# Performance work log

Measured on AMD Instinct MI355X. Metric: run time of the kernel, lower is better.

The kernel has to match this reference:

```python
import jax, jax.numpy as jnp
import numpy as np
from jax import lax

B, N, C, FH, FW = 2, 6, 64, 16, 44
D = 64
DEPTH_MIN, DEPTH_MAX = 1.0, 60.0
IMG_H, IMG_W = 256, 704
BEV_H, BEV_W = 128, 128
XMIN, XMAX = -51.2, 51.2
YMIN, YMAX = -51.2, 51.2
BN_EPS = 1e-5


def _make_cameras():
    fx = fy = 557.0
    K = np.array([[fx, 0.0, IMG_W / 2.0], [0.0, fy, IMG_H / 2.0], [0.0, 0.0, 1.0]], np.float32)
    intr = np.broadcast_to(K, (B, N, 3, 3)).copy()
    extr = np.zeros((B, N, 4, 4), np.float32)
    for n in range(N):
        c, s = np.cos(2 * np.pi * n / N), np.sin(2 * np.pi * n / N)
        # columns = [right, down, forward] of camera expressed in ego frame
        Rc = np.array([[s, 0.0, c], [-c, 0.0, s], [0.0, -1.0, 0.0]], np.float32)
        extr[:, n, :3, :3] = Rc
        extr[:, n, :3, 3] = np.array([c, s, 1.5], np.float32)
        extr[:, n, 3, 3] = 1.0
    return jnp.asarray(intr), jnp.asarray(extr)


def _frustum():
    # (D, FH, FW, 3) holding (u*d, v*d, d) in original-image pixel coords
    ds = jnp.linspace(DEPTH_MIN, DEPTH_MAX, D)[:, None, None]
    xs = jnp.linspace(0.0, IMG_W - 1.0, FW)[None, None, :]
    ys = jnp.linspace(0.0, IMG_H - 1.0, FH)[None, :, None]
    d = jnp.broadcast_to(ds, (D, FH, FW))
    x = jnp.broadcast_to(xs, (D, FH, FW))
    y = jnp.broadcast_to(ys, (D, FH, FW))
    return jnp.stack([x * d, y * d, d], axis=-1)


def _conv(x, w, b, pad):
    y = lax.conv_general_dilated(x, w, (1, 1), pad, dimension_numbers=("NCHW", "OIHW", "NCHW"))
    return y + b[None, :, None, None]


def setup_inputs() -> dict:
    key = jax.random.key(0)
    k0, k1, k2 = jax.random.split(key, 3)
    intr, extr = _make_cameras()
    return {
        "features": jax.random.normal(k0, (B, N, C, FH, FW), jnp.float32),
        "intrinsics": intr,
        "extrinsics": extr,
        "conv1_w": jax.random.normal(k1, (C, C, 3, 3), jnp.float32) / np.sqrt(C * 9.0).astype(np.float32),
        "conv1_b": jnp.zeros((C,), jnp.float32),
        "bn_gamma": jnp.ones((C,), jnp.float32),
        "bn_beta": jnp.zeros((C,), jnp.float32),
        "bn_mean": jnp.zeros((C,), jnp.float32),
        "bn_var": jnp.ones((C,), jnp.float32),
        "conv2_w": jax.random.normal(k2, (D, C, 1, 1), jnp.float32) / np.sqrt(float(C)).astype(np.float32),
        "conv2_b": jnp.zeros((D,), jnp.float32),
    }


def reference(features, intrinsics, extrinsics, conv1_w, conv1_b, bn_gamma, bn_beta, bn_mean, bn_var, conv2_w, conv2_b):
    Bv, Nv, Cv, fH, fW = features.shape
    x = features.reshape(Bv * Nv, Cv, fH, fW)

    # DepthNet: conv3x3 -> BN (inference form) -> ReLU -> conv1x1 -> softmax over depth bins
    h = _conv(x, conv1_w, conv1_b, "SAME")
    scale = (bn_gamma / jnp.sqrt(bn_var + BN_EPS))[None, :, None, None]
    h = (h - bn_mean[None, :, None, None]) * scale + bn_beta[None, :, None, None]
    h = jax.nn.relu(h)
    depth = jax.nn.softmax(_conv(h, conv2_w, conv2_b, "VALID"), axis=1)  # (B*N, D, fH, fW)

    # Lift: outer product of features with depth distribution
    volume = x[:, :, None] * depth[:, None]  # (B*N, C, D, fH, fW)

    # Unproject frustum to ego frame for every camera
    pts = _frustum()  # (D, fH, fW, 3)
    Kinv = jnp.linalg.inv(intrinsics)  # (B, N, 3, 3)
    cam = jnp.einsum("bnij,dhwj->bndhwi", Kinv, pts)
    R = extrinsics[..., :3, :3]
    t = extrinsics[..., :3, 3]
    ego = jnp.einsum("bnij,bndhwj->bndhwi", R, cam) + t[:, :, None, None, None, :]

    # BEV voxel indices; invalid points routed to an overflow bucket that is dropped
    ix = jnp.floor((ego[..., 0] - XMIN) / (XMAX - XMIN) * BEV_W).astype(jnp.int32)
    iy = jnp.floor((ego[..., 1] - YMIN) / (YMAX - YMIN) * BEV_H).astype(jnp.int32)
    valid = (ix >= 0) & (ix < BEV_W) & (iy >= 0) & (iy < BEV_H)
    idx = jnp.where(valid, iy * BEV_W + ix, BEV_H * BEV_W)  # (B, N, D, fH, fW)

    # Splat: scatter-add over all cameras/depths/pixels per batch element
    vol = volume.reshape(Bv, Nv, Cv, -1).transpose(0, 2, 1, 3).reshape(Bv, Cv, -1)  # (B, C, N*D*fH*fW)
    idxb = idx.reshape(Bv, -1)

    def pool(v, i):
        return jnp.zeros((Cv, BEV_H * BEV_W + 1), v.dtype).at[:, i].add(v)[:, :-1]

    return jax.vmap(pool)(vol, idxb).reshape(Bv, Cv, BEV_H, BEV_W)
```

## Files before the change

### kernel.cpp

```cpp
#include <hip/hip_runtime.h>
#include <hip/hip_bf16.h>
#include <math.h>

#define B_  2
#define N_  6
#define C_  64
#define FH_ 16
#define FW_ 44
#define D_  64
#define PIX (FH_*FW_)
#define BNI (B_*N_)
#define NPILLAR (BNI*PIX)
#define NPOINT (NPILLAR*D_)
#define BEVH 128
#define BEVW 128
#define BEVC (BEVH*BEVW)
#define NCELL (B_*BEVC)
#define PW 46
#define PP (18*PW)

typedef unsigned int u32;

__device__ __forceinline__ int rlane_i(int v, int l) {
    return __builtin_amdgcn_readlane(v, l);
}
__device__ __forceinline__ float rlane_f(float v, int l) {
    return __int_as_float(__builtin_amdgcn_readlane(__float_as_int(v), l));
}

__global__ __launch_bounds__(256) void k_init_conv(const float* __restrict__ feat,
                                                   const float* __restrict__ w1,
                                                   float* __restrict__ hpAll,
                                                   float* __restrict__ x_t,
                                                   const float* __restrict__ w2,
                                                   float* __restrict__ w2t,
                                                   u32* __restrict__ counts,
                                                   u32* __restrict__ gcursor,
                                                   const float* __restrict__ intr,
                                                   const float* __restrict__ extr,
                                                   double* __restrict__ Mbuf) {
    const int blk = blockIdx.x;
    const int tid = threadIdx.x;

    __shared__ float smem[16 * PP];

    if (blk < 768) {
        if (blk < 128) counts[blk * 256 + tid] = 0u;

        const int bn = blk >> 6;
        const int ch = (blk >> 4) & 3;
        const int o0 = (blk & 15) * 4;
        const int c0 = ch * 16;

        for (int t = tid; t < 4 * PP; t += 256)
            ((float4*)smem)[t] = make_float4(0.f, 0.f, 0.f, 0.f);
        __syncthreads();

        const float4* fb4 = (const float4*)(feat + ((size_t)bn * C_ + c0) * PIX);
#pragma unroll
        for (int k = 0; k < 11; ++k) {
            const int j = k * 256 + tid;
            const int pl = j / 176;
            const int r  = j % 176;
            const int row = r / 11, q = r % 11;
            const float4 v = fb4[j];
            float* dstp = &smem[pl * PP + (row + 1) * PW + q * 4 + 1];
            dstp[0] = v.x; dstp[1] = v.y; dstp[2] = v.z; dstp[3] = v.w;
        }
        __syncthreads();

        const int y0 = tid / FW_,          x0 = tid % FW_;
        const int y1 = (tid + 256) / FW_,  x1 = (tid + 256) % FW_;
        const int y2 = (tid + 512) / FW_,  x2 = (tid + 512) % FW_;
        const int rp0 = y0 * PW + x0;
        const int rp1 = y1 * PW + x1;
        const int rp2 = y2 * PW + x2;

        float a00=0,a01=0,a02=0,a03=0, a10=0,a11=0,a12=0,a13=0,
              a20=0,a21=0,a22=0,a23=0;
#pragma unroll 4
        for (int i = 0; i < 16; ++i) {
            const float* wr0 = w1 + ((size_t)(o0 + 0) * C_ + c0 + i) * 9;
            const float* wr1 = w1 + ((size_t)(o0 + 1) * C_ + c0 + i) * 9;
            const float* wr2 = w1 + ((size_t)(o0 + 2) * C_ + c0 + i) * 9;
            const float* wr3 = w1 + ((size_t)(o0 + 3) * C_ + c0 + i) * 9;
            const float* pb = &smem[i * PP];
#define CONV_SLOT(RP, A0, A1, A2, A3)                                          \
    {                                                                          \
        const float* bb = pb + (RP);                                           \
        const float n0=bb[0], n1=bb[1], n2=bb[2];                              \
        const float n3=bb[PW], n4=bb[PW+1], n5=bb[PW+2];                       \
        const float n6=bb[2*PW], n7=bb[2*PW+1], n8=bb[2*PW+2];                 \
        A0 += n0*wr0[0]+n1*wr0[1]+n2*wr0[2]+n3*wr0[3]+n4*wr0[4]                \
            + n5*wr0[5]+n6*wr0[6]+n7*wr0[7]+n8*wr0[8];                         \
        A1 += n0*wr1[0]+n1*wr1[1]+n2*wr1[2]+n3*wr1[3]+n4*wr1[4]                \
            + n5*wr1[5]+n6*wr1[6]+n7*wr1[7]+n8*wr1[8];                         \
        A2 += n0*wr2[0]+n1*wr2[1]+n2*wr2[2]+n3*wr2[3]+n4*wr2[4]                \
            + n5*wr2[5]+n6*wr2[6]+n7*wr2[7]+n8*wr2[8];                         \
        A3 += n0*wr3[0]+n1*wr3[1]+n2*wr3[2]+n3*wr3[3]+n4*wr3[4]                \
            + n5*wr3[5]+n6*wr3[6]+n7*wr3[7]+n8*wr3[8];                         \
    }
            CONV_SLOT(rp0, a00, a01, a02, a03);
            CONV_SLOT(rp1, a10, a11, a12, a13);
            if (tid < PIX - 512) CONV_SLOT(rp2, a20, a21, a22, a23);
#undef CONV_SLOT
        }
        float* hp = hpAll + (size_t)ch * NPOINT + (size_t)bn * PIX * C_;
        *(float4*)&hp[(size_t)tid * C_ + o0]         = make_float4(a00,a01,a02,a03);
        *(float4*)&hp[(size_t)(tid + 256) * C_ + o0] = make_float4(a10,a11,a12,a13);
        if (tid < PIX - 512)
            *(float4*)&hp[(size_t)(tid + 512) * C_ + o0] = make_float4(a20,a21,a22,a23);
    } else if (blk < 900) {
        const int u  = blk - 768;
        const int bn = u / 11;
        const int p0 = (u % 11) * 64;
        const int lane = tid & 63;
        const int row4 = tid >> 6;
        float* tile = smem;
#pragma unroll
        for (int k = 0; k < 16; ++k) {
            const int c = k * 4 + row4;
            tile[c * 65 + lane] = feat[((size_t)bn * C_ + c) * PIX + p0 + lane];
        }
        __syncthreads();
#pragma unroll
        for (int k = 0; k < 16; ++k) {
            const int r = k * 4 + row4;
            x_t[((size_t)bn * PIX + p0 + r) * C_ + lane] = tile[lane * 65 + r];
        }
    } else {
#pragma unroll
        for (int k = 0; k < 16; ++k) {
            const int idx = k * 256 + tid;
            const int d = idx >> 6, c = idx & 63;
            w2t[c * D_ + d] = w2[idx];
        }
        if (tid == 0) *gcursor = 0u;
        if (tid < BNI) {
            const float* K = &intr[tid * 9];
            const double a00 = K[0], a01 = K[1], a02 = K[2];
            const double a10 = K[3], a11 = K[4], a12 = K[5];
            const double a20 = K[6], a21 = K[7], a22 = K[8];
            const double det = a00 * (a11 * a22 - a12 * a21)
                             - a01 * (a10 * a22 - a12 * a20)
                             + a02 * (a10 * a21 - a11 * a20);
            const double id = 1.0 / det;
            double inv[9];
            inv[0] = (a11 * a22 - a12 * a21) * id;
            inv[1] = (a02 * a21 - a01 * a22) * id;
            inv[2] = (a01 * a12 - a02 * a11) * id;
            inv[3] = (a12 * a20 - a10 * a22) * id;
            inv[4] = (a00 * a22 - a02 * a20) * id;
            inv[5] = (a02 * a10 - a00 * a12) * id;
            inv[6] = (a10 * a21 - a11 * a20) * id;
            inv[7] = (a01 * a20 - a00 * a21) * id;
            inv[8] = (a00 * a11 - a01 * a10) * id;
            const float* E = &extr[tid * 16];
            double* M = &Mbuf[tid * 9];
            for (int r = 0; r < 3; ++r) {
                const double r0 = E[r*4+0], r1 = E[r*4+1], r2 = E[r*4+2];
                M[r*3+0] = r0*inv[0] + r1*inv[3] + r2*inv[6];
                M[r*3+1] = r0*inv[1] + r1*inv[4] + r2*inv[7];
                M[r*3+2] = r0*inv[2] + r1*inv[5] + r2*inv[8];
            }
        }
    }
}

__global__ __launch_bounds__(256) void k_depth(const float* __restrict__ hpAll,
                                               const float* __restrict__ b1,
                                               const float* __restrict__ gma,
                                               const float* __restrict__ bta,
                                               const float* __restrict__ mu,
                                               const float* __restrict__ var,
                                               const float* __restrict__ w2t,
                                               const float* __restrict__ b2,
                                               const double* __restrict__ Mbuf,
                                               const float* __restrict__ extr,
                                               uint2* __restrict__ pc,
                                               u32* __restrict__ counts) {
    const int wv = threadIdx.x >> 6;
    const int d  = threadIdx.x & 63;
    const int pillar = blockIdx.x * 4 + wv;
    const int bn = pillar / PIX;
    const int p  = pillar % PIX;
    const int yi = p / FW_;
    const int xi = p % FW_;

    __shared__ float hs[4][C_];
    {
        const size_t o = (size_t)pillar * C_ + d;
        float h = hpAll[o] + hpAll[NPOINT + o] + hpAll[2 * (size_t)NPOINT + o]
                + hpAll[3 * (size_t)NPOINT + o] + b1[d];
        const float sc = gma[d] / sqrtf(var[d] + 1e-5f);
        h = (h - mu[d]) * sc + bta[d];
        hs[wv][d] = h > 0.f ? h : 0.f;
    }
    __syncthreads();

    float logit = b2[d];
#pragma unroll
    for (int c = 0; c < C_; ++c) logit += hs[wv][c] * w2t[c * D_ + d];

    float m = logit;
#pragma unroll
    for (int off = 32; off; off >>= 1) m = fmaxf(m, __shfl_xor(m, off));
    float e = expf(logit - m);
    float s = e;
#pragma unroll
    for (int off = 32; off; off >>= 1) s += __shfl_xor(s, off);

    const double* M = &Mbuf[bn * 9];
    const double xn = (double)xi * (703.0 / 43.0);
    const double yn = (double)yi * 17.0;
    const double vx = M[0] * xn + M[1] * yn + M[2];
    const double vy = M[3] * xn + M[4] * yn + M[5];
    const double dd = 1.0 + (double)d * (59.0 / 63.0);
    const float* E = &extr[bn * 16];
    const double ex = dd * vx + (double)E[3];
    const double ey = dd * vy + (double)E[7];
    const int ix = (int)floor((ex + 51.2) * 1.25);
    const int iy = (int)floor((ey + 51.2) * 1.25);
    const bool valid = (ix >= 0) && (ix < BEVW) && (iy >= 0) && (iy < BEVH);

    const int i = pillar * D_ + d;
    uint2 rec;
    rec.x = __float_as_uint(e / s);
    if (valid) {
        const int cell = (bn / N_) * BEVC + iy * BEVW + ix;
        const u32 rank = atomicAdd(&counts[cell], 1u);
        rec.y = (rank << 15) | (u32)cell;
    } else {
        rec.y = 0xFFFFFFFFu;
    }
    pc[i] = rec;
}

__global__ __launch_bounds__(256) void k_alloc(const u32* __restrict__ counts,
                                               u32* __restrict__ offs,
                                               u32* __restrict__ gcursor) {
    const int cell = blockIdx.x * 256 + threadIdx.x;
    const int lane = threadIdx.x & 63;
    const u32 len = counts[cell];
    u32 incl = len;
#pragma unroll
    for (int off = 1; off < 64; off <<= 1) {
        u32 t = __shfl_up(incl, off);
        if (lane >= off) incl += t;
    }
    u32 base = 0;
    if (lane == 63) base = atomicAdd(gcursor, incl);
    base = (u32)__shfl((int)base, 63);
    offs[cell] = base + incl - len;
}

__global__ __launch_bounds__(256) void k_zero_place(const uint2* __restrict__ pc,
                                                    const u32* __restrict__ offs,
                                                    const u32* __restrict__ counts,
                                                    const u32* __restrict__ gcursor,
                                                    uint2* __restrict__ sorted,
                                                    u32* __restrict__ offs_end,
                                                    float* __restrict__ out) {
    const int blk = blockIdx.x;
    const int tid = threadIdx.x;
    if (blk < 2048) {
        const int gt = blk * 256 + tid;
        const int c4 = gt & 4095;
        const int bc = gt >> 12;
        const int b  = bc >> 6;
        const int cellbase = b * BEVC + (c4 << 2);
        const uint4 s4 = *(const uint4*)&offs[cellbase];
        const uint4 n4 = *(const uint4*)&counts[cellbase];
        float* dst = out + ((size_t)bc * BEVC) + (c4 << 2);
        if ((n4.x | n4.y | n4.z | n4.w) == 0u) {
            *(float4*)dst = make_float4(0.f, 0.f, 0.f, 0.f);
        } else {
            if (n4.x == 0u || (s4.x >> 6) != ((s4.x + n4.x - 1) >> 6)) dst[0] = 0.f;
            if (n4.y == 0u || (s4.y >> 6) != ((s4.y + n4.y - 1) >> 6)) dst[1] = 0.f;
            if (n4.z == 0u || (s4.z >> 6) != ((s4.z + n4.z - 1) >> 6)) dst[2] = 0.f;
            if (n4.w == 0u || (s4.w >> 6) != ((s4.w + n4.w - 1) >> 6)) dst[3] = 0.f;
        }
    } else if (blk < 4160) {
        const int i = (blk - 2048) * 256 + tid;
        const uint2 rec = pc[i];
        if (rec.y != 0xFFFFFFFFu) {
            const u32 cell = rec.y & 0x7FFFu;
            const u32 rank = rec.y >> 15;
            const u32 pos  = offs[cell] + rank;
            uint2 o; o.x = rec.x; o.y = (cell << 14) | (u32)(i >> 6);
            sorted[pos] = o;
        }
    } else {
        const u32 total = *gcursor;
        if (tid < 128) {
            uint2 dummy; dummy.x = 0u; dummy.y = 0xFFFFFFFFu;
            sorted[total + tid] = dummy;
        }
        if (tid == 128) *offs_end = total;
    }
}

__global__ __launch_bounds__(256) void k_pool(const uint2* __restrict__ sorted,
                                              const u32* __restrict__ offsets,
                                              const float* __restrict__ x_t,
                                              float* __restrict__ out) {
    const u32 P = offsets[NCELL];
    const int wv   = threadIdx.x >> 6;
    const int lane = threadIdx.x & 63;
    const u32 j0   = ((u32)blockIdx.x * 4u + (u32)wv) * 64u;
    if (j0 >= P) return;

    const uint2 pr  = sorted[j0 + (u32)lane];
    const float myw = __uint_as_float(pr.x);
    const int mycell = (int)(pr.y >> 14);
    int mypil = (int)(pr.y & 0x3FFFu);
    if (mypil >= NPILLAR) mypil = 0;

    const int prev_cell = (j0 > 0) ? (int)(sorted[j0 - 1].y >> 14) : -1;
    const int next_cell = (int)(sorted[j0 + 64].y >> 14);

    const int upc = __shfl_up(mycell, 1);
    const unsigned long long bm = __ballot(lane == 0 || mycell != upc);

    float xr[8];
#pragma unroll
    for (int t = 0; t < 8; ++t)
        xr[t] = x_t[(size_t)rlane_i(mypil, t) * C_ + lane];

    float acc = 0.f;
    bool first = true;

#pragma unroll
    for (int t = 0; t < 64; ++t) {
        acc += rlane_f(myw, t) * xr[t & 7];
        if (t + 8 < 64)
            xr[t & 7] = x_t[(size_t)rlane_i(mypil, t + 8) * C_ + lane];
        const bool flush = (t == 63) || ((bm >> (t + 1)) & 1ull);
        if (flush) {
            const int cc = rlane_i(mycell, t);
            if (cc < NCELL) {
                float* dst = out + ((size_t)(cc >> 14) * C_ + lane) * BEVC
                           + (cc & (BEVC - 1));
                const bool spans = (first && cc == prev_cell)
                                || (t == 63 && next_cell == cc);
                if (spans) atomicAdd(dst, acc);
                else *dst = acc;
            }
            acc = 0.f;
            first = false;
        }
    }
}

extern "C" void kernel_launch(void* const* d_in, const int* in_sizes, int n_in,
                              void* d_out, int out_size, void* d_ws, size_t ws_size,
                              hipStream_t stream) {
    const float* feat  = (const float*)d_in[0];
    const float* intr  = (const float*)d_in[1];
    const float* extr  = (const float*)d_in[2];
    const float* w1    = (const float*)d_in[3];
    const float* b1    = (const float*)d_in[4];
    const float* gma   = (const float*)d_in[5];
    const float* bta   = (const float*)d_in[6];
    const float* mu    = (const float*)d_in[7];
    const float* var   = (const float*)d_in[8];
    const float* w2    = (const float*)d_in[9];
    const float* b2    = (const float*)d_in[10];
    float* out = (float*)d_out;

    double* Mbuf    = (double*)d_ws;
    u32*    gcursor = (u32*)((char*)d_ws + 960);
    uint2*  sorted  = (uint2*)((char*)d_ws + 1024);
    uint2*  pc      = sorted + NPOINT + 128;
    float*  x_t     = (float*)(pc + NPOINT);
    float*  hpAll   = x_t + NPOINT;
    u32*    counts  = (u32*)(hpAll + 4 * (size_t)NPOINT);
    u32*    offs    = counts + NCELL;
    float*  w2t     = (float*)(offs + NCELL + 1);

    k_init_conv<<<901, 256, 0, stream>>>(feat, w1, hpAll, x_t, w2, w2t,
                                         counts, gcursor, intr, extr, Mbuf);
    k_depth<<<NPILLAR / 4, 256, 0, stream>>>(hpAll, b1, gma, bta, mu, var,
                                             w2t, b2, Mbuf, extr, pc, counts);
    k_alloc<<<NCELL / 256, 256, 0, stream>>>(counts, offs, gcursor);
    k_zero_place<<<4161, 256, 0, stream>>>(pc, offs, counts, gcursor,
                                           sorted, &offs[NCELL], out);
    k_pool<<<NPOINT / 64 / 4, 256, 0, stream>>>(sorted, offs, x_t, out);

    (void)in_sizes; (void)n_in; (void)ws_size; (void)out_size;
}
```

Measured before the change: 106.6 us.

## Pool into cell-major scratch buffer and transpose to channel-major output

The pooling kernel now writes each cell's 64 channels contiguously into a cell-major scratch buffer that reuses the hpAll workspace, instead of scattering one float per channel with a 64KB stride in the NCHW output. A new kernel transposes that buffer into the channel-major output through a padded shared-memory tile. The zeroing pass is reworked to clear the scratch rows per cell. This is meant to coalesce the pool writes and atomics, at the cost of an extra kernel launch and a full read and write of the output-sized buffer.

```diff
diff --git a/kernel.cpp b/kernel.cpp
--- a/kernel.cpp
+++ b/kernel.cpp
@@ -260,26 +260,19 @@
                                                     const u32* __restrict__ gcursor,
                                                     uint2* __restrict__ sorted,
                                                     u32* __restrict__ offs_end,
-                                                    float* __restrict__ out) {
+                                                    float* __restrict__ spool) {
     const int blk = blockIdx.x;
     const int tid = threadIdx.x;
     if (blk < 2048) {
         const int gt = blk * 256 + tid;
-        const int c4 = gt & 4095;
-        const int bc = gt >> 12;
-        const int b  = bc >> 6;
-        const int cellbase = b * BEVC + (c4 << 2);
-        const uint4 s4 = *(const uint4*)&offs[cellbase];
-        const uint4 n4 = *(const uint4*)&counts[cellbase];
-        float* dst = out + ((size_t)bc * BEVC) + (c4 << 2);
-        if ((n4.x | n4.y | n4.z | n4.w) == 0u) {
-            *(float4*)dst = make_float4(0.f, 0.f, 0.f, 0.f);
-        } else {
-            if (n4.x == 0u || (s4.x >> 6) != ((s4.x + n4.x - 1) >> 6)) dst[0] = 0.f;
-            if (n4.y == 0u || (s4.y >> 6) != ((s4.y + n4.y - 1) >> 6)) dst[1] = 0.f;
-            if (n4.z == 0u || (s4.z >> 6) != ((s4.z + n4.z - 1) >> 6)) dst[2] = 0.f;
-            if (n4.w == 0u || (s4.w >> 6) != ((s4.w + n4.w - 1) >> 6)) dst[3] = 0.f;
-        }
+        const int cell = gt >> 4;
+        const int q    = gt & 15;
+        const u32 n = counts[cell];
+        const u32 s = offs[cell];
+        const bool needzero = (n == 0u) || ((s >> 6) != ((s + n - 1) >> 6));
+        if (needzero)
+            *(float4*)&spool[(size_t)cell * C_ + q * 4] =
+                make_float4(0.f, 0.f, 0.f, 0.f);
     } else if (blk < 4160) {
         const int i = (blk - 2048) * 256 + tid;
         const uint2 rec = pc[i];
@@ -303,7 +296,7 @@
 __global__ __launch_bounds__(256) void k_pool(const uint2* __restrict__ sorted,
                                               const u32* __restrict__ offsets,
                                               const float* __restrict__ x_t,
-                                              float* __restrict__ out) {
+                                              float* __restrict__ spool) {
     const u32 P = offsets[NCELL];
     const int wv   = threadIdx.x >> 6;
     const int lane = threadIdx.x & 63;
@@ -339,8 +332,7 @@
         if (flush) {
             const int cc = rlane_i(mycell, t);
             if (cc < NCELL) {
-                float* dst = out + ((size_t)(cc >> 14) * C_ + lane) * BEVC
-                           + (cc & (BEVC - 1));
+                float* dst = spool + (size_t)cc * C_ + lane;
                 const bool spans = (first && cc == prev_cell)
                                 || (t == 63 && next_cell == cc);
                 if (spans) atomicAdd(dst, acc);
@@ -349,6 +341,29 @@
             acc = 0.f;
             first = false;
         }
+    }
+}
+
+__global__ __launch_bounds__(256) void k_out(const float* __restrict__ spool,
+                                             float* __restrict__ out) {
+    const int tile_i = blockIdx.x;
+    const int b  = tile_i >> 8;
+    const int c0 = (tile_i & 255) * 64;
+    const int tid = threadIdx.x;
+    const int lane = tid & 63;
+    const int row4 = tid >> 6;
+
+    __shared__ float tile[64][65];
+#pragma unroll
+    for (int k = 0; k < 16; ++k) {
+        const int r = k * 4 + row4;
+        tile[r][lane] = spool[((size_t)b * BEVC + c0 + r) * C_ + lane];
+    }
+    __syncthreads();
+#pragma unroll
+    for (int k = 0; k < 16; ++k) {
+        const int ch = k * 4 + row4;
+        out[((size_t)b * C_ + ch) * BEVC + c0 + lane] = tile[lane][ch];
     }
 }
 
@@ -378,14 +393,17 @@
     u32*    offs    = counts + NCELL;
     float*  w2t     = (float*)(offs + NCELL + 1);
 
+    float*  spool   = hpAll;
+
     k_init_conv<<<901, 256, 0, stream>>>(feat, w1, hpAll, x_t, w2, w2t,
                                          counts, gcursor, intr, extr, Mbuf);
     k_depth<<<NPILLAR / 4, 256, 0, stream>>>(hpAll, b1, gma, bta, mu, var,
                                              w2t, b2, Mbuf, extr, pc, counts);
     k_alloc<<<NCELL / 256, 256, 0, stream>>>(counts, offs, gcursor);
     k_zero_place<<<4161, 256, 0, stream>>>(pc, offs, counts, gcursor,
-                                           sorted, &offs[NCELL], out);
-    k_pool<<<NPOINT / 64 / 4, 256, 0, stream>>>(sorted, offs, x_t, out);
+                                           sorted, &offs[NCELL], spool);
+    k_pool<<<NPOINT / 64 / 4, 256, 0, stream>>>(sorted, offs, x_t, spool);
+    k_out<<<512, 256, 0, stream>>>(spool, out);
 
     (void)in_sizes; (void)n_in; (void)ws_size; (void)out_size;
 }
```

Result: faster. 89.31 us (-16.2%).
